# Kernel optimization log

Hardware: AMD Instinct MI355X
Metric: run time of the kernel (lower is better)

## Reference

```python
import jax, jax.numpy as jnp
import numpy as np

B, T, D = 16, 2048, 768


def sinusoidal_pe(t, d, dtype):
    # standard transformer sinusoidal positional encoding [t, d]
    pos = jnp.arange(t, dtype=jnp.float32)[:, None]            # [t,1]
    i = jnp.arange(d // 2, dtype=jnp.float32)[None, :]          # [1,d/2]
    ang = pos / jnp.power(10000.0, 2.0 * i / d)                 # [t,d/2]
    pe = jnp.concatenate([jnp.sin(ang), jnp.cos(ang)], axis=-1) # [t,d]
    return pe.astype(dtype)


def setup_inputs() -> dict:
    key = jax.random.key(0)
    k1, k2, k3 = jax.random.split(key, 3)
    wav_features = jax.random.normal(k1, (B, T, D), dtype=jnp.float32)
    # right-aligned padding: per-sample valid lengths in [T//2, T]
    lens = jax.random.randint(k2, (B,), T // 2, T + 1)
    feature_padding_mask = jnp.arange(T)[None, :] >= lens[:, None]       # [B,T] bool
    # patchout mask: Bernoulli(0.5) over frames (the masker)
    non_visible_mask = jax.random.bernoulli(k3, 0.5, (B, T))             # [B,T] bool
    return {
        "wav_features": wav_features,
        "non_visible_mask": non_visible_mask,
        "feature_padding_mask": feature_padding_mask,
    }


def reference(wav_features, non_visible_mask, feature_padding_mask):
    # training-path mask(): add PE, then per-row compact the visible,
    # non-padded frames to the front (ragged gather), zero-pad the rest.
    b, t, d = wav_features.shape
    to_mask = wav_features + sinusoidal_pe(t, d, wav_features.dtype)[None]  # [B,T,D]
    keep = jnp.logical_and(~non_visible_mask, ~feature_padding_mask)        # [B,T]
    # stable argsort on ~keep puts kept indices first, in original order ==
    # prefix-sum-offset gather (torch boolean-index semantics)
    order = jnp.argsort(~keep, axis=1, stable=True)                         # [B,T]
    visible = jnp.take_along_axis(to_mask, order[:, :, None], axis=1)       # [B,T,D]
    visible_lens = keep.sum(axis=1)                                          # [B]
    visible_padding_mask = jnp.arange(t)[None, :] >= visible_lens[:, None]  # [B,T]
    # torch pads ragged rows with zeros; we pad to static T (>= maxlen) for jit
    visible = jnp.where(visible_padding_mask[:, :, None],
                        jnp.zeros((), visible.dtype), visible)
    return visible, visible_padding_mask, visible_lens
```

## Files before the change

### kernel.cpp

```cpp
#include <hip/hip_runtime.h>

#define BB 16
#define TT 2048
#define DD 768

typedef float f32x4 __attribute__((ext_vector_type(4)));

__global__ void pm_scan_kernel(const int* __restrict__ nonvis,
                               const int* __restrict__ pad,
                               int* __restrict__ src_idx,
                               int* __restrict__ lens,
                               float* __restrict__ out_mask,
                               float* __restrict__ out_lens) {
    const int b = blockIdx.x;
    const int tid = threadIdx.x;
    const int base_t = tid * 8;
    const int lane = tid & 63;
    const int wid = tid >> 6;

    const int4* nv4 = reinterpret_cast<const int4*>(nonvis + b * TT) + tid * 2;
    const int4* pd4 = reinterpret_cast<const int4*>(pad + b * TT) + tid * 2;
    const int4 nva = nv4[0], nvb = nv4[1];
    const int4 pda = pd4[0], pdb = pd4[1];

    int keep[8];
    keep[0] = (nva.x == 0) && (pda.x == 0);
    keep[1] = (nva.y == 0) && (pda.y == 0);
    keep[2] = (nva.z == 0) && (pda.z == 0);
    keep[3] = (nva.w == 0) && (pda.w == 0);
    keep[4] = (nvb.x == 0) && (pdb.x == 0);
    keep[5] = (nvb.y == 0) && (pdb.y == 0);
    keep[6] = (nvb.z == 0) && (pdb.z == 0);
    keep[7] = (nvb.w == 0) && (pdb.w == 0);

    int cnt = 0;
#pragma unroll
    for (int k = 0; k < 8; ++k) cnt += keep[k];

    int x = cnt;
#pragma unroll
    for (int off = 1; off < 64; off <<= 1) {
        const int v = __shfl_up(x, off);
        if (lane >= off) x += v;
    }

    __shared__ int wtot[4];
    if (lane == 63) wtot[wid] = x;
    __syncthreads();

    const int t0 = wtot[0], t1 = wtot[1], t2 = wtot[2], t3 = wtot[3];
    const int total = t0 + t1 + t2 + t3;
    int wbase = 0;
    if (wid > 0) wbase += t0;
    if (wid > 1) wbase += t1;
    if (wid > 2) wbase += t2;

    const int incl = wbase + x;
    int pos = incl - cnt;

    int* si = src_idx + b * TT;
#pragma unroll
    for (int k = 0; k < 8; ++k) {
        if (keep[k]) {
            si[pos] = base_t + k;
            ++pos;
        }
    }

    float m[8];
#pragma unroll
    for (int k = 0; k < 8; ++k) m[k] = (base_t + k >= total) ? 1.0f : 0.0f;
    float4* om4 = reinterpret_cast<float4*>(out_mask + b * TT) + tid * 2;
    om4[0] = make_float4(m[0], m[1], m[2], m[3]);
    om4[1] = make_float4(m[4], m[5], m[6], m[7]);

    if (tid == 0) {
        lens[b] = total;
        out_lens[b] = (float)total;
    }
}

__global__ void pm_gather_kernel(const float* __restrict__ wav,
                                 const int* __restrict__ src_idx,
                                 const int* __restrict__ lens,
                                 float* __restrict__ out) {
    const int lane = threadIdx.x & 63;
    const int wid  = threadIdx.x >> 6;
    const int row  = blockIdx.x * 4 + wid;
    const int j = row & (TT - 1);
    const int b = row >> 11;

    f32x4* orow = reinterpret_cast<f32x4*>(out + (size_t)row * DD);

    if (j < lens[b]) {
        const int t = src_idx[b * TT + j];
        const f32x4* arow =
            reinterpret_cast<const f32x4*>(wav + ((size_t)(b * TT + t)) * DD);
        const float tf = (float)t;
#pragma unroll
        for (int s = 0; s < 3; ++s) {
            const int d4 = lane + s * 64;
            const f32x4 a = arow[d4];
            const int d0 = d4 * 4;
            f32x4 v;
#pragma unroll
            for (int k = 0; k < 4; ++k) {
                const int d = d0 + k;
                const int i = (d < DD / 2) ? d : (d - DD / 2);
                const float inv = __expf(-0.0239852613853510f * (float)i);
                const float ang = tf * inv;
                const float pe = (d < DD / 2) ? __sinf(ang) : __cosf(ang);
                v[k] = a[k] + pe;
            }
            __builtin_nontemporal_store(v, orow + d4);
        }
    } else {
        const f32x4 z = {0.f, 0.f, 0.f, 0.f};
#pragma unroll
        for (int s = 0; s < 3; ++s)
            __builtin_nontemporal_store(z, orow + lane + s * 64);
    }
}

extern "C" void kernel_launch(void* const* d_in, const int* in_sizes, int n_in,
                              void* d_out, int out_size, void* d_ws, size_t ws_size,
                              hipStream_t stream) {
    const float* wav   = (const float*)d_in[0];
    const int* nonvis  = (const int*)d_in[1];
    const int* pad     = (const int*)d_in[2];

    float* out       = (float*)d_out;
    float* out_vis   = out;
    float* out_mask  = out + (size_t)BB * TT * DD;
    float* out_lens  = out_mask + BB * TT;

    int* src_idx = (int*)d_ws;
    int* lens    = src_idx + BB * TT;

    pm_scan_kernel<<<BB, 256, 0, stream>>>(nonvis, pad, src_idx, lens,
                                           out_mask, out_lens);

    pm_gather_kernel<<<BB * TT / 4, 256, 0, stream>>>(wav, src_idx, lens, out_vis);
}
```

Baseline: 28.54 us.

## Fuse mask scan into gather kernel with per-block redundant prefix scan

Replaces the separate scan and gather kernels with one kernel. Each block of 16 output rows recomputes the full row prefix scan of the keep mask and scatters only its own 16 source indices into shared memory, then gathers and adds the positional encoding. This removes a kernel launch, the dependency between the two kernels and the workspace round trip for the indices. In exchange, each of the 128 blocks per batch row rereads the 2048-entry masks and redoes the scan.

```diff
diff --git a/kernel.cpp b/kernel.cpp
--- a/kernel.cpp
+++ b/kernel.cpp
@@ -6,13 +6,15 @@
 
 typedef float f32x4 __attribute__((ext_vector_type(4)));
 
-__global__ void pm_scan_kernel(const int* __restrict__ nonvis,
-                               const int* __restrict__ pad,
-                               int* __restrict__ src_idx,
-                               int* __restrict__ lens,
-                               float* __restrict__ out_mask,
-                               float* __restrict__ out_lens) {
-    const int b = blockIdx.x;
+__global__ void pm_fused_kernel(const int* __restrict__ nonvis,
+                                const int* __restrict__ pad,
+                                const float* __restrict__ wav,
+                                float* __restrict__ out_vis,
+                                float* __restrict__ out_mask,
+                                float* __restrict__ out_lens) {
+    const int blk = blockIdx.x;
+    const int b = blk >> 7;
+    const int j0 = (blk & 127) << 4;
     const int tid = threadIdx.x;
     const int base_t = tid * 8;
     const int lane = tid & 63;
@@ -45,6 +47,7 @@
     }
 
     __shared__ int wtot[4];
+    __shared__ int s_src[16];
     if (lane == 63) wtot[wid] = x;
     __syncthreads();
 
@@ -55,70 +58,66 @@
     if (wid > 1) wbase += t1;
     if (wid > 2) wbase += t2;
 
-    const int incl = wbase + x;
-    int pos = incl - cnt;
+    int p = wbase + x - cnt;
 
-    int* si = src_idx + b * TT;
 #pragma unroll
     for (int k = 0; k < 8; ++k) {
         if (keep[k]) {
-            si[pos] = base_t + k;
-            ++pos;
+            const int r = p - j0;
+            if ((unsigned)r < 16u) s_src[r] = base_t + k;
+            ++p;
         }
     }
+    __syncthreads();
 
-    float m[8];
+    if (tid < 16)
+        out_mask[b * TT + j0 + tid] = (j0 + tid >= total) ? 1.0f : 0.0f;
+    if ((blk & 127) == 0 && tid == 0)
+        out_lens[b] = (float)total;
+
+    float invf[3];
+    bool is_sin[3];
 #pragma unroll
-    for (int k = 0; k < 8; ++k) m[k] = (base_t + k >= total) ? 1.0f : 0.0f;
-    float4* om4 = reinterpret_cast<float4*>(out_mask + b * TT) + tid * 2;
-    om4[0] = make_float4(m[0], m[1], m[2], m[3]);
-    om4[1] = make_float4(m[4], m[5], m[6], m[7]);
+    for (int s = 0; s < 3; ++s) {
+        const int d0 = (lane + s * 64) * 4;
+        is_sin[s] = (d0 < DD / 2);
+        (void)invf;
+    }
 
-    if (tid == 0) {
-        lens[b] = total;
-        out_lens[b] = (float)total;
-    }
-}
+#pragma unroll
+    for (int q = 0; q < 4; ++q) {
+        const int r = wid * 4 + q;
+        const int j = j0 + r;
+        f32x4* orow = reinterpret_cast<f32x4*>(out_vis + ((size_t)(b * TT + j)) * DD);
 
-__global__ void pm_gather_kernel(const float* __restrict__ wav,
-                                 const int* __restrict__ src_idx,
-                                 const int* __restrict__ lens,
-                                 float* __restrict__ out) {
-    const int lane = threadIdx.x & 63;
-    const int wid  = threadIdx.x >> 6;
-    const int row  = blockIdx.x * 4 + wid;
-    const int j = row & (TT - 1);
-    const int b = row >> 11;
-
-    f32x4* orow = reinterpret_cast<f32x4*>(out + (size_t)row * DD);
-
-    if (j < lens[b]) {
-        const int t = src_idx[b * TT + j];
-        const f32x4* arow =
-            reinterpret_cast<const f32x4*>(wav + ((size_t)(b * TT + t)) * DD);
-        const float tf = (float)t;
+        if (j < total) {
+            const int t = s_src[r];
+            const f32x4* arow =
+                reinterpret_cast<const f32x4*>(wav + ((size_t)(b * TT + t)) * DD);
+            const float tf = (float)t;
 #pragma unroll
-        for (int s = 0; s < 3; ++s) {
-            const int d4 = lane + s * 64;
-            const f32x4 a = arow[d4];
-            const int d0 = d4 * 4;
-            f32x4 v;
+            for (int s = 0; s < 3; ++s) {
+                const int d4 = lane + s * 64;
+                const f32x4 a = arow[d4];
+                const int d0 = d4 * 4;
+                f32x4 v;
 #pragma unroll
-            for (int k = 0; k < 4; ++k) {
-                const int d = d0 + k;
-                const int i = (d < DD / 2) ? d : (d - DD / 2);
-                const float inv = __expf(-0.0239852613853510f * (float)i);
-                const float ang = tf * inv;
-                const float pe = (d < DD / 2) ? __sinf(ang) : __cosf(ang);
-                v[k] = a[k] + pe;
+                for (int k = 0; k < 4; ++k) {
+                    const int d = d0 + k;
+                    const int i = is_sin[s] ? d : (d - DD / 2);
+                    const float inv = __expf(-0.0239852613853510f * (float)i);
+                    const float ang = tf * inv;
+                    const float pe = is_sin[s] ? __sinf(ang) : __cosf(ang);
+                    v[k] = a[k] + pe;
+                }
+                __builtin_nontemporal_store(v, orow + d4);
             }
-            __builtin_nontemporal_store(v, orow + d4);
+        } else {
+            const f32x4 z = {0.f, 0.f, 0.f, 0.f};
+#pragma unroll
+            for (int s = 0; s < 3; ++s)
+                __builtin_nontemporal_store(z, orow + lane + s * 64);
         }
-    } else {
-        const f32x4 z = {0.f, 0.f, 0.f, 0.f};
-#pragma unroll
-        for (int s = 0; s < 3; ++s)
-            __builtin_nontemporal_store(z, orow + lane + s * 64);
     }
 }
 
@@ -134,11 +133,6 @@
     float* out_mask  = out + (size_t)BB * TT * DD;
     float* out_lens  = out_mask + BB * TT;
 
-    int* src_idx = (int*)d_ws;
-    int* lens    = src_idx + BB * TT;
-
-    pm_scan_kernel<<<BB, 256, 0, stream>>>(nonvis, pad, src_idx, lens,
-                                           out_mask, out_lens);
-
-    pm_gather_kernel<<<BB * TT / 4, 256, 0, stream>>>(wav, src_idx, lens, out_vis);
+    pm_fused_kernel<<<BB * TT / 16, 256, 0, stream>>>(nonvis, pad, wav,
+                                                      out_vis, out_mask, out_lens);
 }
```

After: 25.76 us. 9.7% less time.
